# Kernel tuning notes

Hardware: AMD Instinct MI355X
Metric: run time of the kernel (lower is better)

Reference implementation:

```python
import math
import jax, jax.numpy as jnp
import numpy as np

ROUNDS = 4
BUCKET_LEN = 64
NEG_BIG = -1e9
NEG_SELF = -1e5
EPS = 1e-12


def look_back(x):
    # x: [B, n_buckets, bucket_len, ...]; prepend previous bucket (circular) along bucket_len axis
    return jnp.concatenate([jnp.roll(x, 1, axis=1), x], axis=2)


def gather_dim1(x, idx):
    # torch expand_gather: broadcast x and idx to common shape, gather along axis 1
    shape = np.broadcast_shapes(x.shape, idx.shape)
    return jnp.take_along_axis(jnp.broadcast_to(x, shape), jnp.broadcast_to(idx, shape), axis=1)


def setup_inputs() -> dict:
    key = jax.random.key(0)
    k1, k2, k3 = jax.random.split(key, 3)
    B, L, d_k = 16, 4096, 64
    n_buckets = L // BUCKET_LEN
    query = jax.random.normal(k1, (B, L, d_k), dtype=jnp.float32)
    value = jax.random.normal(k2, (B, L, d_k), dtype=jnp.float32)
    rand_matrix = jax.random.normal(k3, (B, d_k, ROUNDS, n_buckets // 2), dtype=jnp.float32)
    return {"query": query, "value": value, "rand_matrix": rand_matrix, "seed": 0}


def lsh_hashes(query, rand_matrix):
    # LocalitySensitiveHash.forward
    B, L, d_k = query.shape
    qn = query / jnp.maximum(jnp.linalg.norm(query, axis=-1, keepdims=True), EPS)
    rm = rand_matrix / jnp.linalg.norm(rand_matrix, axis=1, keepdims=True)
    mm = jnp.einsum('bld,bdrn->blrn', qn, rm)  # [B, L, rounds, n_buckets//2]
    h = jnp.argmax(jnp.concatenate([mm, -mm], axis=-1), axis=-1).astype(jnp.int32)  # [B, L, rounds]
    return h * L + jnp.arange(L, dtype=jnp.int32)[None, :, None]  # unique per position


def _lsh_attention(query, value, rand_matrix):
    B, L, d_k = query.shape
    R, bl = ROUNDS, BUCKET_LEN
    nb = L // bl

    h = lsh_hashes(query, rand_matrix)
    sorted_hashes = jnp.sort(h, axis=1)
    hash_indice = jnp.argsort(h, axis=1)               # [B, L, R]
    original_indice = jnp.argsort(hash_indice, axis=1)  # reverse_sort

    # reorder queries by hash, bucketize: [B, nb, bl, d_k, R]
    rq = gather_dim1(query[:, :, :, None], hash_indice[:, :, None, :]).reshape(B, nb, bl, d_k, R)
    lb_key = look_back(rq)
    lb_key = lb_key / jnp.maximum(jnp.linalg.norm(lb_key, axis=-2, keepdims=True), EPS)
    scores = jnp.einsum('bnidr,bnjdr->bnijr', rq, lb_key) / math.sqrt(d_k)  # [B, nb, bl, 2bl, R]

    # mask: different buckets, causal, self
    sh = sorted_hashes.reshape(B, nb, bl, R) // L  # bucket id
    scores = jnp.where(sh[..., None, :] != look_back(sh)[..., None, :, :], NEG_BIG, scores)
    qi = hash_indice.reshape(B, nb, bl, R).astype(jnp.int32)
    ki = look_back(qi)  # [B, nb, 2bl, R]
    scores = jnp.where(qi[..., None, :] < ki[..., None, :, :], NEG_BIG, scores)
    scores = jnp.where(qi[..., None, :] == ki[..., None, :, :], NEG_SELF, scores)

    # duplicate-key counting across rounds (get_dup_keys)
    ki_full = jnp.broadcast_to(ki[:, :, None, :, :], (B, nb, bl, 2 * bl, R)).reshape(B, L, 2 * bl, R)
    ki_full = gather_dim1(ki_full, original_indice[:, :, None, :])
    flat = ki_full.reshape(B, L, 2 * bl * R)
    s_idx = jnp.argsort(flat, axis=-1)
    s = jnp.take_along_axis(flat, s_idx, axis=-1)
    counts = jnp.ones_like(s)
    for i in range(1, R):
        eq = (s[..., i:] == s[..., :-i]).astype(s.dtype)
        counts = counts + jnp.pad(eq, ((0, 0), (0, 0), (i, 0))) + jnp.pad(eq, ((0, 0), (0, 0), (0, i)))
    inv = jnp.argsort(s_idx, axis=-1)
    count_key = jnp.take_along_axis(counts, inv, axis=-1).reshape(B, L, 2 * bl, R)
    count_key = gather_dim1(count_key, hash_indice[:, :, None, :])

    # duplicate-adjusted softmax
    scores = scores.reshape(B, L, 2 * bl, R)
    lse = jax.nn.logsumexp(scores, axis=2)  # [B, L, R]
    softmax_qk = jnp.exp(scores - jnp.log(count_key.astype(scores.dtype)) - lse[:, :, None, :])

    rv = gather_dim1(value[:, :, :, None], hash_indice[:, :, None, :]).reshape(B, nb, bl, d_k, R)
    sm = softmax_qk.reshape(B, nb, bl, 2 * bl, R)
    attn = jnp.einsum('bnijr,bnjdr->bnidr', sm, look_back(rv)).reshape(B, L, d_k, R)
    attn = gather_dim1(attn, original_indice[:, :, None, :])
    lse = jnp.take_along_axis(lse, original_indice, axis=1)
    round_weights = jax.nn.softmax(lse, axis=1)  # dim=1 (length) exactly as in the source
    return jnp.einsum('bldr,blr->bld', attn, round_weights)


def reference(query, value, rand_matrix, seed):
    # seed is unused by the original forward body; dropout skipped (eval mode)
    return _lsh_attention(query, value, rand_matrix)
```

## Files before the change

kernel.cpp:

```cpp
#include <hip/hip_runtime.h>
#include <math.h>

#define B_  16
#define L_  4096
#define D_  64
#define R_  4
#define NB_ 64
#define BL_ 64
#define FIXCAP 8192

typedef _Float16 f16x8 __attribute__((ext_vector_type(8)));
typedef _Float16 f16x2 __attribute__((ext_vector_type(2)));
typedef float    f32x4 __attribute__((ext_vector_type(4)));


__global__ __launch_bounds__(64) void k_rmnorm(const float* __restrict__ rm,
                                               double* __restrict__ rmn,
                                               _Float16* __restrict__ rhi_g,
                                               _Float16* __restrict__ rlo_g,
                                               int* __restrict__ fix_cnt) {
    if (blockIdx.x == 0 && threadIdx.x == 0) *fix_cnt = 0;
    int blk = blockIdx.x;
    int b = blk >> 7, r = (blk >> 5) & 3, n = blk & 31;
    int d = threadIdx.x;
    double v = (double)rm[(((size_t)b * 64 + d) * 4 + r) * 32 + n];
    double sq = v * v;
    #pragma unroll
    for (int off = 32; off > 0; off >>= 1) sq += __shfl_down(sq, off);
    double tot = __shfl(sq, 0);
    double nv = v / sqrt(tot);
    rmn[(((size_t)b * 4 + r) * 32 + n) * 64 + d] = nv;
    float f = (float)nv;
    _Float16 hi = (_Float16)f;
    size_t gi = ((size_t)b * 128 + r * 32 + n) * 64 + d;
    rhi_g[gi] = hi;
    rlo_g[gi] = (_Float16)(f - (float)hi);
}

__global__ __launch_bounds__(256) void k_prep(const float* __restrict__ q,
                                              const float* __restrict__ value,
                                              _Float16* __restrict__ qhf,
                                              _Float16* __restrict__ khf,
                                              _Float16* __restrict__ vhf) {
    int xcd = blockIdx.x & 7, slot = blockIdx.x >> 3;
    int b = xcd * 2 + (slot >> 6), chunk = slot & 63;
    int t = threadIdx.x;
    int row = chunk * 64 + (t >> 2), sub = t & 3;
    size_t off = ((size_t)(b * L_ + row)) * 64 + sub * 16;

    const float4* qp = (const float4*)(q + off);
    float qv[16];
    #pragma unroll
    for (int c = 0; c < 4; c++) {
        float4 tt = qp[c];
        qv[4*c+0]=tt.x; qv[4*c+1]=tt.y; qv[4*c+2]=tt.z; qv[4*c+3]=tt.w;
    }
    float ss = 0.f;
    #pragma unroll
    for (int j = 0; j < 16; j++) ss += qv[j] * qv[j];
    ss += __shfl_xor(ss, 1);
    ss += __shfl_xor(ss, 2);
    float nr = sqrtf(ss); if (nr < 1e-12f) nr = 1e-12f;
    float kscale = 0.125f / nr;
    f16x8 qh0, qh1, kh0, kh1;
    #pragma unroll
    for (int j = 0; j < 8; j++) {
        qh0[j] = (_Float16)qv[j];            qh1[j] = (_Float16)qv[8+j];
        kh0[j] = (_Float16)(qv[j] * kscale); kh1[j] = (_Float16)(qv[8+j] * kscale);
    }
    *(f16x8*)(qhf + off) = qh0; *(f16x8*)(qhf + off + 8) = qh1;
    *(f16x8*)(khf + off) = kh0; *(f16x8*)(khf + off + 8) = kh1;

    const float4* vp = (const float4*)(value + off);
    float vv[16];
    #pragma unroll
    for (int c = 0; c < 4; c++) {
        float4 tt = vp[c];
        vv[4*c+0]=tt.x; vv[4*c+1]=tt.y; vv[4*c+2]=tt.z; vv[4*c+3]=tt.w;
    }
    f16x8 vh0, vh1;
    #pragma unroll
    for (int j = 0; j < 8; j++) { vh0[j]=(_Float16)vv[j]; vh1[j]=(_Float16)vv[8+j]; }
    *(f16x8*)(vhf + off) = vh0; *(f16x8*)(vhf + off + 8) = vh1;
}

__global__ __launch_bounds__(256, 4) void k_hash(const float* __restrict__ q,
                                                 const _Float16* __restrict__ rhi_g,
                                                 const _Float16* __restrict__ rlo_g,
                                                 int* __restrict__ h_ws,
                                                 int* __restrict__ fix_cnt,
                                                 int* __restrict__ fix_list) {
    __shared__ __align__(16) char smem[36864];
    _Float16* Rhi = (_Float16*)smem;
    _Float16* Rlo = (_Float16*)(smem + 18432);
    float*    Sc  = (float*)smem;

    int xcd = blockIdx.x & 7, slot = blockIdx.x >> 3;
    int b = xcd * 2 + (slot >> 6), chunk = slot & 63;
    int tid = threadIdx.x;
    int w = tid >> 6, lane = tid & 63, quad = lane >> 4, l15 = lane & 15;

    {
        int row = tid >> 1, dh = (tid & 1) * 32;
        const _Float16* sh = rhi_g + ((size_t)b * 128 + row) * 64 + dh;
        const _Float16* sl = rlo_g + ((size_t)b * 128 + row) * 64 + dh;
        #pragma unroll
        for (int g = 0; g < 4; g++) {
            *(f16x8*)&Rhi[row * 72 + dh + g * 8] = *(const f16x8*)(sh + g * 8);
            *(f16x8*)&Rlo[row * 72 + dh + g * 8] = *(const f16x8*)(sl + g * 8);
        }
    }

    int qrow = chunk * 64 + w * 16 + l15;
    const float* qp = q + ((size_t)(b * L_ + qrow)) * 64;
    f16x8 Ahi[2], Alo[2];
    #pragma unroll
    for (int kt = 0; kt < 2; kt++) {
        float4 t0 = *(const float4*)(qp + kt * 32 + quad * 8);
        float4 t1 = *(const float4*)(qp + kt * 32 + quad * 8 + 4);
        float fv[8] = {t0.x, t0.y, t0.z, t0.w, t1.x, t1.y, t1.z, t1.w};
        #pragma unroll
        for (int j = 0; j < 8; j++) {
            _Float16 hi = (_Float16)fv[j];
            Ahi[kt][j] = hi;
            Alo[kt][j] = (_Float16)(fv[j] - (float)hi);
        }
    }
    __syncthreads();

    f32x4 acc[8];
    #pragma unroll
    for (int jt = 0; jt < 8; jt++) acc[jt] = (f32x4){0.f, 0.f, 0.f, 0.f};
    #pragma unroll
    for (int jt = 0; jt < 8; jt++) {
        #pragma unroll
        for (int kt = 0; kt < 2; kt++) {
            f16x8 bh = *(const f16x8*)&Rhi[(jt * 16 + l15) * 72 + kt * 32 + quad * 8];
            f16x8 bl = *(const f16x8*)&Rlo[(jt * 16 + l15) * 72 + kt * 32 + quad * 8];
            acc[jt] = __builtin_amdgcn_mfma_f32_16x16x32_f16(Ahi[kt], bh, acc[jt], 0, 0, 0);
            acc[jt] = __builtin_amdgcn_mfma_f32_16x16x32_f16(Ahi[kt], bl, acc[jt], 0, 0, 0);
            acc[jt] = __builtin_amdgcn_mfma_f32_16x16x32_f16(Alo[kt], bh, acc[jt], 0, 0, 0);
        }
    }
    __syncthreads();

    #pragma unroll
    for (int jt = 0; jt < 8; jt++) {
        #pragma unroll
        for (int reg = 0; reg < 4; reg++)
            Sc[(w * 16 + quad * 4 + reg) * 133 + jt * 16 + l15] = acc[jt][reg];
    }
    __syncthreads();

    {
        int row = tid & 63, r = tid >> 6;
        const float* sp = &Sc[row * 133 + r * 32];
        float bp = -1e30f, bn = -1e30f; int ip = 0, in2 = 0;
        float v1 = -1e30f, v2 = -1e30f;
        #pragma unroll
        for (int n = 0; n < 32; n++) {
            float v = sp[n], nv = -v;
            if (v > bp)  { bp = v;  ip = n; }
            if (nv > bn) { bn = nv; in2 = n; }
            if (v > v1)       { v2 = v1; v1 = v; }
            else if (v > v2)  { v2 = v; }
            if (nv > v1)      { v2 = v1; v1 = nv; }
            else if (nv > v2) { v2 = nv; }
        }
        int i1 = (bp >= bn) ? ip : (32 + in2);
        int l = chunk * 64 + row;
        h_ws[((size_t)(b * 4 + r)) * L_ + l] = i1;
        if (v1 - v2 < 4e-5f) {
            int slot2 = atomicAdd(fix_cnt, 1);
            if (slot2 < FIXCAP) fix_list[slot2] = (b << 14) | (r << 12) | l;
        }
    }
}

__global__ __launch_bounds__(64) void k_fix(const float* __restrict__ q,
                                            const double* __restrict__ rmn,
                                            const int* __restrict__ fix_cnt,
                                            const int* __restrict__ fix_list,
                                            int* __restrict__ h_ws) {
    int cnt = *fix_cnt; if (cnt > FIXCAP) cnt = FIXCAP;
    int lane = threadIdx.x;
    for (int i = blockIdx.x; i < cnt; i += gridDim.x) {
        int e = fix_list[i];
        int b = e >> 14, r = (e >> 12) & 3, l = e & 4095;
        int n = lane & 31;
        const double* rp = rmn + ((size_t)(b * 4 + r)) * 2048 + n * 64;
        const float* qr = q + ((size_t)(b * L_ + l)) * 64;
        double a0 = 0.0, a1 = 0.0, a2 = 0.0, a3 = 0.0;
        #pragma unroll
        for (int d = 0; d < 64; d += 4) {
            a0 += (double)qr[d]   * rp[d];
            a1 += (double)qr[d+1] * rp[d+1];
            a2 += (double)qr[d+2] * rp[d+2];
            a3 += (double)qr[d+3] * rp[d+3];
        }
        double acc = ((a0 + a1) + (a2 + a3));
        double v = (lane < 32) ? acc : -acc;
        int idx = lane;
        #pragma unroll
        for (int off = 1; off < 64; off <<= 1) {
            double ov = __shfl_xor(v, off);
            int   oidx = __shfl_xor(idx, off);
            if (ov > v || (ov == v && oidx < idx)) { v = ov; idx = oidx; }
        }
        if (lane == 0) h_ws[((size_t)(b * 4 + r)) * L_ + l] = idx;
    }
}

__global__ __launch_bounds__(256) void k_sort(const int* __restrict__ h_ws,
                                              int* __restrict__ hi_ws,
                                              int* __restrict__ oi_ws) {
    __shared__ unsigned short hs16[4096];
    __shared__ unsigned short cnt[256 * 66];
    __shared__ int partial[4 * 64];
    __shared__ int baseb[64];
    int br = blockIdx.x;
    const int* hp = h_ws + (size_t)br * L_;
    int t = threadIdx.x;
    for (int k = t; k < 4096; k += 256) hs16[k] = (unsigned short)hp[k];
    for (int k = t; k < 256 * 66; k += 256) cnt[k] = 0;
    __syncthreads();
    {
        unsigned short* row = &cnt[t * 66];
        int base = t * 16;
        #pragma unroll
        for (int k = 0; k < 16; k++) row[hs16[base + k]]++;
    }
    __syncthreads();
    {
        int u = t & 63, g = t >> 6;
        int s = 0;
        for (int c = g * 64; c < g * 64 + 64; c++) s += cnt[c * 66 + u];
        partial[g * 64 + u] = s;
    }
    __syncthreads();
    if (t < 64) {
        int tot = partial[t] + partial[64 + t] + partial[128 + t] + partial[192 + t];
        int v = tot;
        #pragma unroll
        for (int off = 1; off < 64; off <<= 1) {
            int u2 = __shfl_up(v, off);
            if (t >= off) v += u2;
        }
        baseb[t] = v - tot;
    }
    __syncthreads();
    {
        int u = t & 63, g = t >> 6;
        int running = baseb[u];
        for (int gg = 0; gg < g; gg++) running += partial[gg * 64 + u];
        for (int c = g * 64; c < g * 64 + 64; c++) {
            int tmp = cnt[c * 66 + u];
            cnt[c * 66 + u] = (unsigned short)running;
            running += tmp;
        }
    }
    __syncthreads();
    {
        int* hi = hi_ws + (size_t)br * L_;
        int* oi = oi_ws + (size_t)br * L_;
        unsigned short* row = &cnt[t * 66];
        int base = t * 16;
        #pragma unroll
        for (int k = 0; k < 16; k++) {
            int idx = base + k;
            int bucket = hs16[idx];
            int pos = row[bucket]++;
            hi[pos] = idx;
            oi[idx] = pos;
        }
    }
}

__global__ __launch_bounds__(256) void k_meta(const int* __restrict__ h_ws,
                                              const int* __restrict__ hi_ws,
                                              const int* __restrict__ oi_ws,
                                              int4* __restrict__ meta_ws) {
    int gid = blockIdx.x * 256 + threadIdx.x;
    int br = gid >> 12, spos = gid & 4095;
    int b = br >> 2;
    int p = hi_ws[(size_t)br * L_ + spos];
    int hh = h_ws[(size_t)br * L_ + p];
    int pack = 0, packm1 = 0;
    #pragma unroll
    for (int r2 = 0; r2 < 4; r2++) {
        int bk = oi_ws[((size_t)(b * 4 + r2)) * L_ + p] >> 6;
        pack   |= bk << (8 * r2);
        packm1 |= ((bk + 63) & 63) << (8 * r2);
    }
    meta_ws[(size_t)br * L_ + spos] = make_int4(hh, p, pack, packm1);
}

__global__ __launch_bounds__(256, 4) void k_attn(const _Float16* __restrict__ qhf,
                                                 const _Float16* __restrict__ khf,
                                                 const _Float16* __restrict__ vhf,
                                                 const int4* __restrict__ meta_ws,
                                                 float* __restrict__ lse_ws,
                                                 _Float16* __restrict__ attn_ws,
                                                 int b_base) {
    __shared__ _Float16 Ksh[128 * 76];
    __shared__ _Float16 Vt[64 * 136];
    __shared__ int4 kmeta[128];

    int xcd = blockIdx.x & 7, slot = blockIdx.x >> 3;
    int b = b_base + xcd;
    int n = slot >> 2, r = slot & 3;
    int tid = threadIdx.x;
    int w = tid >> 6, lane = tid & 63, quad = lane >> 4, l15 = lane & 15;
    int hibase = (b * 4 + r) * L_;

    if (tid < 128) {
        int nprev = (n + 63) & 63;
        int spos = (tid < 64) ? (nprev * 64 + tid) : (n * 64 + (tid - 64));
        kmeta[tid] = meta_ws[hibase + spos];
    }
    __syncthreads();

    {
        int j = tid >> 1, dh = (tid & 1) * 32;
        const _Float16* src = khf + ((size_t)(b * L_ + kmeta[j].y)) * 64 + dh;
        #pragma unroll
        for (int g = 0; g < 4; g++)
            *(f16x8*)&Ksh[j * 76 + dh + g * 8] = *(const f16x8*)(src + g * 8);
    }
    {
        int p0 = kmeta[2 * lane].y, p1 = kmeta[2 * lane + 1].y;
        const _Float16* v0 = vhf + ((size_t)(b * L_ + p0)) * 64 + w * 16;
        const _Float16* v1 = vhf + ((size_t)(b * L_ + p1)) * 64 + w * 16;
        f16x8 a00 = *(const f16x8*)v0, a01 = *(const f16x8*)(v0 + 8);
        f16x8 a10 = *(const f16x8*)v1, a11 = *(const f16x8*)(v1 + 8);
        #pragma unroll
        for (int d = 0; d < 8; d++) {
            f16x2 hv = { a00[d], a10[d] };
            *(f16x2*)&Vt[(w * 16 + d) * 136 + 2 * lane] = hv;
            f16x2 hw = { a01[d], a11[d] };
            *(f16x2*)&Vt[(w * 16 + 8 + d) * 136 + 2 * lane] = hw;
        }
    }

    int4 qmw = kmeta[64 + w * 16 + l15];
    const _Float16* qp = qhf + ((size_t)(b * L_ + qmw.y)) * 64;
    f16x8 afr[2];
    afr[0] = *(const f16x8*)(qp + quad * 8);
    afr[1] = *(const f16x8*)(qp + 32 + quad * 8);
    __syncthreads();

    f32x4 acc[8];
    #pragma unroll
    for (int jt = 0; jt < 8; jt++) acc[jt] = (f32x4){0.f, 0.f, 0.f, 0.f};
    #pragma unroll
    for (int jt = 0; jt < 8; jt++) {
        #pragma unroll
        for (int kt = 0; kt < 2; kt++) {
            f16x8 bfr = *(const f16x8*)&Ksh[(jt * 16 + l15) * 76 + kt * 32 + quad * 8];
            acc[jt] = __builtin_amdgcn_mfma_f32_16x16x32_f16(afr[kt], bfr, acc[jt], 0, 0, 0);
        }
    }

    int4 qm4[4], km4[8];
    #pragma unroll
    for (int reg = 0; reg < 4; reg++) qm4[reg] = kmeta[64 + w * 16 + quad * 4 + reg];
    #pragma unroll
    for (int jt = 0; jt < 8; jt++) km4[jt] = kmeta[jt * 16 + l15];
    __syncthreads();

    _Float16* Ph = Ksh;
    float lse_r[4];
    #pragma unroll
    for (int reg = 0; reg < 4; reg++) {
        float s[8];
        #pragma unroll
        for (int jt = 0; jt < 8; jt++) {
            float v = acc[jt][reg];
            if (km4[jt].x != qm4[reg].x) v = -1e9f;
            if (qm4[reg].y < km4[jt].y)  v = -1e9f;
            if (qm4[reg].y == km4[jt].y) v = -1e5f;
            s[jt] = v;
        }
        float m = s[0];
        #pragma unroll
        for (int jt = 1; jt < 8; jt++) m = fmaxf(m, s[jt]);
        #pragma unroll
        for (int off = 1; off < 16; off <<= 1) m = fmaxf(m, __shfl_xor(m, off));
        float te[8], sum = 0.f;
        #pragma unroll
        for (int jt = 0; jt < 8; jt++) { te[jt] = __expf(s[jt] - m); sum += te[jt]; }
        #pragma unroll
        for (int off = 1; off < 16; off <<= 1) sum += __shfl_xor(sum, off);
        float inv = __builtin_amdgcn_rcpf(sum);
        lse_r[reg] = m + __logf(sum);
        int i = w * 16 + quad * 4 + reg;
        #pragma unroll
        for (int jt = 0; jt < 8; jt++) {
            int z1 = km4[jt].z ^ qm4[reg].z;
            int z2 = km4[jt].z ^ qm4[reg].w;
            int nz = __popc((z1 + 0x7f7f7f7f) & 0x80808080)
                   + __popc((z2 + 0x7f7f7f7f) & 0x80808080);
            float p = te[jt] * inv * __builtin_amdgcn_rcpf((float)(8 - nz));
            Ph[i * 136 + jt * 16 + l15] = (_Float16)p;
        }
    }
    if (l15 == 0) {
        #pragma unroll
        for (int reg = 0; reg < 4; reg++)
            lse_ws[hibase + qm4[reg].y] = lse_r[reg];
    }
    __syncthreads();

    f32x4 oacc[4];
    #pragma unroll
    for (int nt = 0; nt < 4; nt++) oacc[nt] = (f32x4){0.f, 0.f, 0.f, 0.f};
    #pragma unroll
    for (int kt = 0; kt < 4; kt++) {
        f16x8 pa = *(const f16x8*)&Ph[(w * 16 + l15) * 136 + kt * 32 + quad * 8];
        #pragma unroll
        for (int nt = 0; nt < 4; nt++) {
            f16x8 vb = *(const f16x8*)&Vt[(nt * 16 + l15) * 136 + kt * 32 + quad * 8];
            oacc[nt] = __builtin_amdgcn_mfma_f32_16x16x32_f16(pa, vb, oacc[nt], 0, 0, 0);
        }
    }
    #pragma unroll
    for (int reg = 0; reg < 4; reg++) {
        size_t base = (((size_t)(b * L_ + qm4[reg].y)) * 4 + r) * 64;
        #pragma unroll
        for (int nt = 0; nt < 4; nt++)
            attn_ws[base + nt * 16 + l15] = (_Float16)oacc[nt][reg];
    }
}

__global__ __launch_bounds__(256) void k_rw(const float* __restrict__ lse_ws,
                                            float* __restrict__ rwmax,
                                            float* __restrict__ rwsum) {
    __shared__ float  red[256];
    __shared__ double redd[256];
    int br = blockIdx.x;
    const float* lp = lse_ws + (size_t)br * L_;
    int t = threadIdx.x;
    float m = -1e30f;
    for (int k = t; k < L_; k += 256) m = fmaxf(m, lp[k]);
    red[t] = m; __syncthreads();
    for (int s2 = 128; s2 > 0; s2 >>= 1) {
        if (t < s2) red[t] = fmaxf(red[t], red[t + s2]);
        __syncthreads();
    }
    float mm = red[0];
    double s = 0.0;
    for (int k = t; k < L_; k += 256) s += (double)expf(lp[k] - mm);
    redd[t] = s; __syncthreads();
    for (int s2 = 128; s2 > 0; s2 >>= 1) {
        if (t < s2) redd[t] += redd[t + s2];
        __syncthreads();
    }
    if (t == 0) { rwmax[br] = mm; rwsum[br] = (float)redd[0]; }
}

__global__ __launch_bounds__(256) void k_out(const _Float16* __restrict__ attn_ws,
                                             const float* __restrict__ lse_ws,
                                             const float* __restrict__ rwmax,
                                             const float* __restrict__ rwsum,
                                             float* __restrict__ out) {
    int xcd = blockIdx.x & 7, slot = blockIdx.x >> 3;
    int b = xcd * 2 + (slot >> 7);
    int inner = slot & 127;
    int tid = threadIdx.x;
    int l = inner * 32 + (tid >> 3), g = tid & 7;
    size_t row = (size_t)b * L_ + l;
    float o[8];
    #pragma unroll
    for (int k = 0; k < 8; k++) o[k] = 0.f;
    #pragma unroll
    for (int r = 0; r < 4; r++) {
        int br = b * 4 + r;
        float wgt = __expf(lse_ws[(size_t)br * L_ + l] - rwmax[br])
                  * __builtin_amdgcn_rcpf(rwsum[br]);
        f16x8 av = *(const f16x8*)&attn_ws[(row * 4 + r) * 64 + g * 8];
        #pragma unroll
        for (int k = 0; k < 8; k++) o[k] += (float)av[k] * wgt;
    }
    float4* op = (float4*)(out + row * 64 + g * 8);
    op[0] = make_float4(o[0], o[1], o[2], o[3]);
    op[1] = make_float4(o[4], o[5], o[6], o[7]);
}

extern "C" void kernel_launch(void* const* d_in, const int* in_sizes, int n_in,
                              void* d_out, int out_size, void* d_ws, size_t ws_size,
                              hipStream_t stream) {
    const float* query = (const float*)d_in[0];
    const float* value = (const float*)d_in[1];
    const float* rm    = (const float*)d_in[2];
    char* ws = (char*)d_ws;
    double*    rmn    = (double*)ws;
    int*       h_ws   = (int*)(ws + ((size_t)1 << 20));
    int*       hi_ws  = (int*)(ws + ((size_t)2 << 20));
    int*       oi_ws  = (int*)(ws + ((size_t)3 << 20));
    float*     lse_ws = (float*)(ws + ((size_t)4 << 20));
    float*     rwmax  = (float*)(ws + ((size_t)5 << 20));
    float*     rwsum  = (float*)(ws + ((size_t)5 << 20) + 256);
    int*       fix_cnt= (int*)(ws + ((size_t)5 << 20) + 512);
    int*       fix_list=(int*)(ws + ((size_t)5 << 20) + 1024);
    _Float16*  attn_ws= (_Float16*)(ws + ((size_t)6 << 20));
    _Float16*  rhi_g  = (_Float16*)(ws + ((size_t)40 << 20));
    _Float16*  rlo_g  = (_Float16*)(ws + ((size_t)40 << 20) + ((size_t)1 << 19));
    int4*      meta_ws= (int4*)(ws + ((size_t)41 << 20));
    _Float16*  qhf    = (_Float16*)(ws + ((size_t)45 << 20));
    _Float16*  khf    = (_Float16*)(ws + ((size_t)53 << 20));
    _Float16*  vhf    = (_Float16*)(ws + ((size_t)61 << 20));
    float*     out    = (float*)d_out;

    hipLaunchKernelGGL(k_rmnorm, dim3(2048), dim3(64),  0, stream, rm, rmn, rhi_g, rlo_g, fix_cnt);
    hipLaunchKernelGGL(k_prep,   dim3(1024), dim3(256), 0, stream, query, value, qhf, khf, vhf);
    hipLaunchKernelGGL(k_hash,   dim3(1024), dim3(256), 0, stream, query, rhi_g, rlo_g,
                       h_ws, fix_cnt, fix_list);
    hipLaunchKernelGGL(k_fix,    dim3(64),   dim3(64),  0, stream, query, rmn,
                       fix_cnt, fix_list, h_ws);
    hipLaunchKernelGGL(k_sort,   dim3(64),   dim3(256), 0, stream, h_ws, hi_ws, oi_ws);
    hipLaunchKernelGGL(k_meta,   dim3(1024), dim3(256), 0, stream, h_ws, hi_ws, oi_ws, meta_ws);
    hipLaunchKernelGGL(k_attn,   dim3(2048), dim3(256), 0, stream,
                       qhf, khf, vhf, meta_ws, lse_ws, attn_ws, 0);
    hipLaunchKernelGGL(k_attn,   dim3(2048), dim3(256), 0, stream,
                       qhf, khf, vhf, meta_ws, lse_ws, attn_ws, 8);
    hipLaunchKernelGGL(k_rw,     dim3(64),   dim3(256), 0, stream, lse_ws, rwmax, rwsum);
    hipLaunchKernelGGL(k_out,    dim3(2048), dim3(256), 0, stream,
                       attn_ws, lse_ws, rwmax, rwsum, out);
}
```

Before: 182.8 us.

## Merge rmnorm and prep, fold hash fix into sort, single attention launch

```diff
diff --git a/kernel.cpp b/kernel.cpp
--- a/kernel.cpp
+++ b/kernel.cpp
@@ -14,38 +14,40 @@
 typedef float    f32x4 __attribute__((ext_vector_type(4)));
 
 
-__global__ __launch_bounds__(64) void k_rmnorm(const float* __restrict__ rm,
-                                               double* __restrict__ rmn,
-                                               _Float16* __restrict__ rhi_g,
-                                               _Float16* __restrict__ rlo_g,
-                                               int* __restrict__ fix_cnt) {
-    if (blockIdx.x == 0 && threadIdx.x == 0) *fix_cnt = 0;
-    int blk = blockIdx.x;
-    int b = blk >> 7, r = (blk >> 5) & 3, n = blk & 31;
-    int d = threadIdx.x;
-    double v = (double)rm[(((size_t)b * 64 + d) * 4 + r) * 32 + n];
-    double sq = v * v;
-    #pragma unroll
-    for (int off = 32; off > 0; off >>= 1) sq += __shfl_down(sq, off);
-    double tot = __shfl(sq, 0);
-    double nv = v / sqrt(tot);
-    rmn[(((size_t)b * 4 + r) * 32 + n) * 64 + d] = nv;
-    float f = (float)nv;
-    _Float16 hi = (_Float16)f;
-    size_t gi = ((size_t)b * 128 + r * 32 + n) * 64 + d;
-    rhi_g[gi] = hi;
-    rlo_g[gi] = (_Float16)(f - (float)hi);
-}
-
-__global__ __launch_bounds__(256) void k_prep(const float* __restrict__ q,
+__global__ __launch_bounds__(256) void k_init(const float* __restrict__ rm,
+                                              const float* __restrict__ q,
                                               const float* __restrict__ value,
+                                              double* __restrict__ rmn,
+                                              _Float16* __restrict__ rhi_g,
+                                              _Float16* __restrict__ rlo_g,
                                               _Float16* __restrict__ qhf,
                                               _Float16* __restrict__ khf,
-                                              _Float16* __restrict__ vhf) {
-    int xcd = blockIdx.x & 7, slot = blockIdx.x >> 3;
+                                              _Float16* __restrict__ vhf,
+                                              int* __restrict__ fix_cnt) {
+    int tid = threadIdx.x;
+    if (blockIdx.x == 0 && tid == 0) *fix_cnt = 0;
+    if (blockIdx.x < 512) {
+        int t4 = blockIdx.x * 4 + (tid >> 6);
+        int b = t4 >> 7, r = (t4 >> 5) & 3, n = t4 & 31;
+        int d = tid & 63;
+        double v = (double)rm[(((size_t)b * 64 + d) * 4 + r) * 32 + n];
+        double sq = v * v;
+        #pragma unroll
+        for (int off = 32; off > 0; off >>= 1) sq += __shfl_down(sq, off);
+        double tot = __shfl(sq, 0);
+        double nv = v / sqrt(tot);
+        rmn[(((size_t)b * 4 + r) * 32 + n) * 64 + d] = nv;
+        float f = (float)nv;
+        _Float16 hi = (_Float16)f;
+        size_t gi = ((size_t)b * 128 + r * 32 + n) * 64 + d;
+        rhi_g[gi] = hi;
+        rlo_g[gi] = (_Float16)(f - (float)hi);
+        return;
+    }
+    int blk = blockIdx.x - 512;
+    int xcd = blk & 7, slot = blk >> 3;
     int b = xcd * 2 + (slot >> 6), chunk = slot & 63;
-    int t = threadIdx.x;
-    int row = chunk * 64 + (t >> 2), sub = t & 3;
+    int row = chunk * 64 + (tid >> 2), sub = tid & 3;
     size_t off = ((size_t)(b * L_ + row)) * 64 + sub * 16;
 
     const float4* qp = (const float4*)(q + off);
@@ -177,41 +179,11 @@
     }
 }
 
-__global__ __launch_bounds__(64) void k_fix(const float* __restrict__ q,
-                                            const double* __restrict__ rmn,
-                                            const int* __restrict__ fix_cnt,
-                                            const int* __restrict__ fix_list,
-                                            int* __restrict__ h_ws) {
-    int cnt = *fix_cnt; if (cnt > FIXCAP) cnt = FIXCAP;
-    int lane = threadIdx.x;
-    for (int i = blockIdx.x; i < cnt; i += gridDim.x) {
-        int e = fix_list[i];
-        int b = e >> 14, r = (e >> 12) & 3, l = e & 4095;
-        int n = lane & 31;
-        const double* rp = rmn + ((size_t)(b * 4 + r)) * 2048 + n * 64;
-        const float* qr = q + ((size_t)(b * L_ + l)) * 64;
-        double a0 = 0.0, a1 = 0.0, a2 = 0.0, a3 = 0.0;
-        #pragma unroll
-        for (int d = 0; d < 64; d += 4) {
-            a0 += (double)qr[d]   * rp[d];
-            a1 += (double)qr[d+1] * rp[d+1];
-            a2 += (double)qr[d+2] * rp[d+2];
-            a3 += (double)qr[d+3] * rp[d+3];
-        }
-        double acc = ((a0 + a1) + (a2 + a3));
-        double v = (lane < 32) ? acc : -acc;
-        int idx = lane;
-        #pragma unroll
-        for (int off = 1; off < 64; off <<= 1) {
-            double ov = __shfl_xor(v, off);
-            int   oidx = __shfl_xor(idx, off);
-            if (ov > v || (ov == v && oidx < idx)) { v = ov; idx = oidx; }
-        }
-        if (lane == 0) h_ws[((size_t)(b * 4 + r)) * L_ + l] = idx;
-    }
-}
-
-__global__ __launch_bounds__(256) void k_sort(const int* __restrict__ h_ws,
+__global__ __launch_bounds__(256) void k_sort(const float* __restrict__ q,
+                                              const double* __restrict__ rmn,
+                                              const int* __restrict__ fix_cnt,
+                                              const int* __restrict__ fix_list,
+                                              int* __restrict__ h_ws,
                                               int* __restrict__ hi_ws,
                                               int* __restrict__ oi_ws) {
     __shared__ unsigned short hs16[4096];
@@ -219,10 +191,45 @@
     __shared__ int partial[4 * 64];
     __shared__ int baseb[64];
     int br = blockIdx.x;
-    const int* hp = h_ws + (size_t)br * L_;
+    int* hp = h_ws + (size_t)br * L_;
     int t = threadIdx.x;
+    int wave = t >> 6, lane = t & 63;
     for (int k = t; k < 4096; k += 256) hs16[k] = (unsigned short)hp[k];
     for (int k = t; k < 256 * 66; k += 256) cnt[k] = 0;
+    __syncthreads();
+    {
+        int fcnt = *fix_cnt; if (fcnt > FIXCAP) fcnt = FIXCAP;
+        int b = br >> 2;
+        for (int i = wave; i < fcnt; i += 4) {
+            int e = fix_list[i];
+            if ((e >> 12) != br) continue;
+            int l = e & 4095;
+            int n = lane & 31;
+            const double* rp = rmn + ((size_t)br) * 2048 + n * 64;
+            const float* qr = q + ((size_t)(b * L_ + l)) * 64;
+            double a0 = 0.0, a1 = 0.0, a2 = 0.0, a3 = 0.0;
+            #pragma unroll
+            for (int d = 0; d < 64; d += 4) {
+                a0 += (double)qr[d]   * rp[d];
+                a1 += (double)qr[d+1] * rp[d+1];
+                a2 += (double)qr[d+2] * rp[d+2];
+                a3 += (double)qr[d+3] * rp[d+3];
+            }
+            double acc = ((a0 + a1) + (a2 + a3));
+            double v = (lane < 32) ? acc : -acc;
+            int idx = lane;
+            #pragma unroll
+            for (int off = 1; off < 64; off <<= 1) {
+                double ov = __shfl_xor(v, off);
+                int   oidx = __shfl_xor(idx, off);
+                if (ov > v || (ov == v && oidx < idx)) { v = ov; idx = oidx; }
+            }
+            if (lane == 0) {
+                hs16[l] = (unsigned short)idx;
+                hp[l] = idx;
+            }
+        }
+    }
     __syncthreads();
     {
         unsigned short* row = &cnt[t * 66];
@@ -300,15 +307,14 @@
                                                  const _Float16* __restrict__ vhf,
                                                  const int4* __restrict__ meta_ws,
                                                  float* __restrict__ lse_ws,
-                                                 _Float16* __restrict__ attn_ws,
-                                                 int b_base) {
+                                                 _Float16* __restrict__ attn_ws) {
     __shared__ _Float16 Ksh[128 * 76];
     __shared__ _Float16 Vt[64 * 136];
     __shared__ int4 kmeta[128];
 
     int xcd = blockIdx.x & 7, slot = blockIdx.x >> 3;
-    int b = b_base + xcd;
-    int n = slot >> 2, r = slot & 3;
+    int b = xcd * 2 + (slot >> 8);
+    int rem = slot & 255, n = rem >> 2, r = rem & 3;
     int tid = threadIdx.x;
     int w = tid >> 6, lane = tid & 63, quad = lane >> 4, l15 = lane & 15;
     int hibase = (b * 4 + r) * L_;
@@ -511,18 +517,15 @@
     _Float16*  vhf    = (_Float16*)(ws + ((size_t)61 << 20));
     float*     out    = (float*)d_out;
 
-    hipLaunchKernelGGL(k_rmnorm, dim3(2048), dim3(64),  0, stream, rm, rmn, rhi_g, rlo_g, fix_cnt);
-    hipLaunchKernelGGL(k_prep,   dim3(1024), dim3(256), 0, stream, query, value, qhf, khf, vhf);
+    hipLaunchKernelGGL(k_init,   dim3(1536), dim3(256), 0, stream,
+                       rm, query, value, rmn, rhi_g, rlo_g, qhf, khf, vhf, fix_cnt);
     hipLaunchKernelGGL(k_hash,   dim3(1024), dim3(256), 0, stream, query, rhi_g, rlo_g,
                        h_ws, fix_cnt, fix_list);
-    hipLaunchKernelGGL(k_fix,    dim3(64),   dim3(64),  0, stream, query, rmn,
-                       fix_cnt, fix_list, h_ws);
-    hipLaunchKernelGGL(k_sort,   dim3(64),   dim3(256), 0, stream, h_ws, hi_ws, oi_ws);
+    hipLaunchKernelGGL(k_sort,   dim3(64),   dim3(256), 0, stream, query, rmn,
+                       fix_cnt, fix_list, h_ws, hi_ws, oi_ws);
     hipLaunchKernelGGL(k_meta,   dim3(1024), dim3(256), 0, stream, h_ws, hi_ws, oi_ws, meta_ws);
-    hipLaunchKernelGGL(k_attn,   dim3(2048), dim3(256), 0, stream,
-                       qhf, khf, vhf, meta_ws, lse_ws, attn_ws, 0);
-    hipLaunchKernelGGL(k_attn,   dim3(2048), dim3(256), 0, stream,
-                       qhf, khf, vhf, meta_ws, lse_ws, attn_ws, 8);
+    hipLaunchKernelGGL(k_attn,   dim3(4096), dim3(256), 0, stream,
+                       qhf, khf, vhf, meta_ws, lse_ws, attn_ws);
     hipLaunchKernelGGL(k_rw,     dim3(64),   dim3(256), 0, stream, lse_ws, rwmax, rwsum);
     hipLaunchKernelGGL(k_out,    dim3(2048), dim3(256), 0, stream,
                        attn_ws, lse_ws, rwmax, rwsum, out);
```

New measurement: 175.2 us. 1.04x faster.
